# Optimization experiments

Measured on AMD Instinct MI355X. Metric: run time of the kernel, lower is better.

## Reference

```python
import jax, jax.numpy as jnp
import numpy as np


def _shared_mlp(x, W, s, b):
    # 1x1 conv over channel dim (last axis) + folded BN (scale/shift) + ReLU
    # x: (..., Cin), W: (Cout, Cin), s/b: (Cout,)
    return jax.nn.relu(jnp.einsum('...c,oc->...o', x, W) * s + b)


def setup_inputs() -> dict:
    key = jax.random.key(0)
    ks = jax.random.split(key, 15)
    B, N, K, C = 4, 4096, 32, 64
    D1, D2, DH = 64, 64, 128
    sc = 0.1
    return {
        'xyz': jax.random.normal(ks[0], (B, N, 3), dtype=jnp.float32),
        'features': jax.random.normal(ks[1], (B, C, N), dtype=jnp.float32),
        'idx': jax.random.randint(ks[2], (N, K), 0, N, dtype=jnp.int32),
        'W_gu': jax.random.normal(ks[3], (D1, 6), dtype=jnp.float32) * sc,
        's_gu': jnp.ones((D1,), jnp.float32),
        'b_gu': jax.random.normal(ks[4], (D1,), dtype=jnp.float32) * sc,
        'W_gv': jax.random.normal(ks[5], (D2, C), dtype=jnp.float32) * sc,
        's_gv': jnp.ones((D2,), jnp.float32),
        'b_gv': jax.random.normal(ks[6], (D2,), dtype=jnp.float32) * sc,
        'W_h': jax.random.normal(ks[7], (DH, D1 + D2), dtype=jnp.float32) * sc,
        's_h': jnp.ones((DH,), jnp.float32),
        'b_h': jax.random.normal(ks[8], (DH,), dtype=jnp.float32) * sc,
        'W_f': jax.random.normal(ks[9], (C, DH), dtype=jnp.float32) * sc,
        's_f': jnp.ones((C,), jnp.float32),
        'b_f': jax.random.normal(ks[10], (C,), dtype=jnp.float32) * sc,
    }


def reference(xyz, features, idx, W_gu, s_gu, b_gu, W_gv, s_gv, b_gv,
              W_h, s_h, b_h, W_f, s_f, b_f):
    # xyz: (B,N,3), features: (B,C,N), idx: (N,K) neighbor indices per point
    feats = jnp.swapaxes(features, 1, 2)              # (B,N,C)
    xyz_nb = xyz[:, idx, :]                           # (B,N,K,3) random gather
    feat_nb = feats[:, idx, :]                        # (B,N,K,C)
    K = idx.shape[1]
    center_xyz = jnp.broadcast_to(xyz[:, :, None, :], xyz_nb.shape)
    rel_xyz = jnp.concatenate([center_xyz, xyz_nb], axis=-1)   # (B,N,K,6)
    rel_feat = feat_nb + feats[:, :, None, :]                  # (B,N,K,C)

    gu = _shared_mlp(rel_xyz, W_gu, s_gu, b_gu)       # (B,N,K,D1)
    gv = _shared_mlp(rel_feat, W_gv, s_gv, b_gv)      # (B,N,K,D2)
    fuse = jnp.concatenate([gu, gv], axis=-1)         # (B,N,K,D1+D2)
    h = _shared_mlp(fuse, W_h, s_h, b_h)              # (B,N,K,DH)
    pooled = jnp.mean(h, axis=2)                      # (B,N,DH) mean over K
    out = _shared_mlp(pooled, W_f, s_f, b_f)          # (B,N,C)
    out = jnp.swapaxes(out, 1, 2) + features          # (B,C,N) residual
    return (xyz, out)
```

## Files before the change

### kernel.cpp

```cpp
#include <hip/hip_runtime.h>

#define B_  4
#define N_  4096
#define K_  32
#define C_  64
#define DH_ 128
#define PPB 16

typedef _Float16 half2v __attribute__((ext_vector_type(2)));
typedef _Float16 half8  __attribute__((ext_vector_type(8)));
typedef __fp16   fp16x2 __attribute__((ext_vector_type(2)));
typedef float  floatx16 __attribute__((ext_vector_type(16)));
typedef unsigned int uint_t;

union HU { half2v h; uint_t u; };
union HU2 { fp16x2 h; uint_t u; };

__device__ __forceinline__ uint_t pk2(float a, float b) {
    HU2 x; x.h = __builtin_amdgcn_cvt_pkrtz(a, b);
    return x.u;
}

__global__ __launch_bounds__(256) void k_transforms(
    const float* __restrict__ xyz,
    const float* __restrict__ W_h,
    const float* __restrict__ s_h,
    float* __restrict__ out_xyz,
    _Float16* __restrict__ Bpack)
{
    int e = blockIdx.x * 256 + threadIdx.x;
    if (e < B_*N_*3) { out_xyz[e] = xyz[e]; return; }
    e -= B_*N_*3;
    int j = e & 7, l = (e >> 3) & 63, c = (e >> 9) & 7, ob = e >> 12;
    int o = ob*32 + (l & 31);
    int i = c*16 + (l >> 5)*8 + j;
    Bpack[e] = (_Float16)(W_h[o*DH_ + i] * s_h[o]);
}

__global__ __launch_bounds__(256) void k_pre(
    const float* __restrict__ xyz,
    const float* __restrict__ features,
    const float* __restrict__ W_gv,
    const float* __restrict__ W_gu,
    const float* __restrict__ s_gu, const float* __restrict__ b_gu,
    const float* __restrict__ s_gv, const float* __restrict__ b_gv,
    uint_t* __restrict__ QsH,
    uint_t* __restrict__ PcatH)
{
    const int b  = blockIdx.x >> 6;
    const int n0 = (blockIdx.x & 63) * 64;
    const int t  = threadIdx.x;

    __shared__ __align__(16) float ftile[64 * 66];
    __shared__ __align__(16) float wtile[64 * 68];
    __shared__ float xs[192];
    __shared__ float wgu[384];

    const int nn = t & 63, cq = t >> 6;
#pragma unroll
    for (int r = 0; r < 16; r++) {
        int c = cq * 16 + r;
        ftile[c*66 + nn] = features[(b*C_ + c)*N_ + n0 + nn];
    }
    for (int e = t; e < 64*64; e += 256) {
        int o = e >> 6, c = e & 63;
        wtile[c*68 + o] = W_gv[e];
    }
    if (t < 192) xs[t] = xyz[(b*N_ + n0)*3 + t];
    if (t < 128) { wgu[t] = W_gu[t]; wgu[t+128] = W_gu[t+128]; wgu[t+256] = W_gu[t+256]; }
    __syncthreads();

    const int nt = t & 31, ot = t >> 5;
    const int nl0 = nt * 2, o0 = ot * 8;

    float acc[2][8] = {};
    for (int c = 0; c < 64; c++) {
        const float2 a = *(const float2*)&ftile[c*66 + nl0];
        float wv[8];
        *(float4*)&wv[0] = *(const float4*)&wtile[c*68 + o0];
        *(float4*)&wv[4] = *(const float4*)&wtile[c*68 + o0 + 4];
#pragma unroll
        for (int oo = 0; oo < 8; oo++) {
            acc[0][oo] = fmaf(a.x, wv[oo], acc[0][oo]);
            acc[1][oo] = fmaf(a.y, wv[oo], acc[1][oo]);
        }
    }

    float sgu[8], bgu[8], sgv[8], bgv[8];
    *(float4*)&sgu[0] = *(const float4*)&s_gu[o0]; *(float4*)&sgu[4] = *(const float4*)&s_gu[o0+4];
    *(float4*)&bgu[0] = *(const float4*)&b_gu[o0]; *(float4*)&bgu[4] = *(const float4*)&b_gu[o0+4];
    *(float4*)&sgv[0] = *(const float4*)&s_gv[o0]; *(float4*)&sgv[4] = *(const float4*)&s_gv[o0+4];
    *(float4*)&bgv[0] = *(const float4*)&b_gv[o0]; *(float4*)&bgv[4] = *(const float4*)&b_gv[o0+4];

#pragma unroll
    for (int kk = 0; kk < 2; kk++) {
        const int nl = nl0 + kk;
        const int bn = b*N_ + n0 + nl;
        const float x0 = xs[nl*3], x1 = xs[nl*3+1], x2 = xs[nl*3+2];
        float qv[8], rv[8];
#pragma unroll
        for (int oo = 0; oo < 8; oo++) {
            const int o = o0 + oo;
            qv[oo] = x0*wgu[o*6+0] + x1*wgu[o*6+1] + x2*wgu[o*6+2];
            rv[oo] = x0*wgu[o*6+3] + x1*wgu[o*6+4] + x2*wgu[o*6+5];
        }
        uint4 qa, pa;
        qa.x = pk2(qv[0]*sgu[0]+bgu[0], qv[1]*sgu[1]+bgu[1]);
        qa.y = pk2(qv[2]*sgu[2]+bgu[2], qv[3]*sgu[3]+bgu[3]);
        qa.z = pk2(qv[4]*sgu[4]+bgu[4], qv[5]*sgu[5]+bgu[5]);
        qa.w = pk2(qv[6]*sgu[6]+bgu[6], qv[7]*sgu[7]+bgu[7]);
        pa.x = pk2(rv[0]*sgu[0], rv[1]*sgu[1]);
        pa.y = pk2(rv[2]*sgu[2], rv[3]*sgu[3]);
        pa.z = pk2(rv[4]*sgu[4], rv[5]*sgu[5]);
        pa.w = pk2(rv[6]*sgu[6], rv[7]*sgu[7]);
        *(uint4*)&QsH  [bn*64 + ot*4] = qa;
        *(uint4*)&PcatH[bn*64 + ot*4] = pa;
        qa.x = pk2(acc[kk][0]*sgv[0]+bgv[0], acc[kk][1]*sgv[1]+bgv[1]);
        qa.y = pk2(acc[kk][2]*sgv[2]+bgv[2], acc[kk][3]*sgv[3]+bgv[3]);
        qa.z = pk2(acc[kk][4]*sgv[4]+bgv[4], acc[kk][5]*sgv[5]+bgv[5]);
        qa.w = pk2(acc[kk][6]*sgv[6]+bgv[6], acc[kk][7]*sgv[7]+bgv[7]);
        pa.x = pk2(acc[kk][0]*sgv[0], acc[kk][1]*sgv[1]);
        pa.y = pk2(acc[kk][2]*sgv[2], acc[kk][3]*sgv[3]);
        pa.z = pk2(acc[kk][4]*sgv[4], acc[kk][5]*sgv[5]);
        pa.w = pk2(acc[kk][6]*sgv[6], acc[kk][7]*sgv[7]);
        *(uint4*)&QsH  [bn*64 + 32 + ot*4] = qa;
        *(uint4*)&PcatH[bn*64 + 32 + ot*4] = pa;
    }
}

__global__ __launch_bounds__(256) void k_main(
    const int*      __restrict__ idx,
    const uint_t*   __restrict__ QsH,
    const uint_t*   __restrict__ PcatH,
    const _Float16* __restrict__ Bpack,
    const float*    __restrict__ b_h,
    const float*    __restrict__ W_f,
    const float*    __restrict__ s_f, const float* __restrict__ b_f,
    const float*    __restrict__ features,
    float* __restrict__ outF)
{
    const int t    = threadIdx.x;
    const int w    = t >> 6;
    const int lane = t & 63;
    const int m    = lane & 31;
    const int hh   = lane >> 5;
    const int slot = w >> 1;
    const int oh   = w & 1;

    __shared__ uint_t fuse[2 * 32 * 66];
    __shared__ __align__(16) float pooledAll[PPB * 136];

    half8 Bf[2][8];
#pragma unroll
    for (int ob = 0; ob < 2; ob++)
#pragma unroll
        for (int c = 0; c < 8; c++)
            Bf[ob][c] = *(const half8*)&Bpack[(((oh*2 + ob)*8 + c)*64 + lane)*8];

    const float bh0 = b_h[(oh*2+0)*32 + m];
    const float bh1 = b_h[(oh*2+1)*32 + m];

    const int bnb   = blockIdx.x * PPB;
    const int base0 = bnb & ~(N_ - 1);
    const half2v zero2 = {(_Float16)0.f, (_Float16)0.f};

    for (int rr = 0; rr < PPB/2; rr++) {
        const int bn0 = bnb + rr*2;
        const int jall = idx[((bn0 + hh) & (N_-1))*K_ + m];
        const uint_t qw0 = QsH[(bn0+0)*64 + lane];
        const uint_t qw1 = QsH[(bn0+1)*64 + lane];

        __syncthreads();
#pragma unroll
        for (int it = 0; it < 16; it++) {
            const int rs  = it*4 + w;
            const int sl  = rs >> 5, row = rs & 31;
            const int j   = __shfl(jall, rs);
            const uint_t rp = PcatH[(base0 + j)*64 + lane];
            HU a, p; a.u = sl ? qw1 : qw0; p.u = rp;
            half2v v = a.h + p.h;
            v = __builtin_elementwise_max(v, zero2);
            HU o2; o2.h = v;
            fuse[sl*2112 + row*66 + lane] = o2.u;
        }
        __syncthreads();

        floatx16 acc0 = {}, acc1 = {};
#pragma unroll
        for (int c = 0; c < 8; c++) {
            const int wb = slot*2112 + m*66 + c*8 + hh*4;
            union { uint_t u[4]; half8 h; } av;
            *(uint2*)&av.u[0] = *(const uint2*)&fuse[wb];
            *(uint2*)&av.u[2] = *(const uint2*)&fuse[wb + 2];
            acc0 = __builtin_amdgcn_mfma_f32_32x32x16_f16(av.h, Bf[0][c], acc0, 0, 0, 0);
            acc1 = __builtin_amdgcn_mfma_f32_32x32x16_f16(av.h, Bf[1][c], acc1, 0, 0, 0);
        }

        float v0 = 0.f, v1 = 0.f;
#pragma unroll
        for (int rg = 0; rg < 16; rg++) {
            v0 += fmaxf(acc0[rg] + bh0, 0.f);
            v1 += fmaxf(acc1[rg] + bh1, 0.f);
        }
        v0 += __shfl_xor(v0, 32);
        v1 += __shfl_xor(v1, 32);
        const int nl = rr*2 + slot;
        if (hh == 0) {
            pooledAll[nl*136 + (oh*2+0)*32 + m] = v0;
            pooledAll[nl*136 + (oh*2+1)*32 + m] = v1;
        }
    }
    __syncthreads();

    const int b  = bnb >> 12;
    const int n0 = bnb & (N_ - 1);
    const int c  = t >> 2;
    const int nq = t & 3;

    float acc[4] = {};
    for (int i0 = 0; i0 < DH_; i0 += 4) {
        const float4 wv = *(const float4*)&W_f[c*DH_ + i0];
#pragma unroll
        for (int r = 0; r < 4; r++) {
            const float4 p = *(const float4*)&pooledAll[(nq*4 + r)*136 + i0];
            acc[r] += wv.x*p.x + wv.y*p.y + wv.z*p.z + wv.w*p.w;
        }
    }
    const float sfc = s_f[c] * (1.f/(float)K_);
    const float bfc = b_f[c];
    const float4 fr = *(const float4*)&features[(b*C_ + c)*N_ + n0 + nq*4];
    float4 ov;
    ov.x = fmaxf(acc[0]*sfc + bfc, 0.f) + fr.x;
    ov.y = fmaxf(acc[1]*sfc + bfc, 0.f) + fr.y;
    ov.z = fmaxf(acc[2]*sfc + bfc, 0.f) + fr.z;
    ov.w = fmaxf(acc[3]*sfc + bfc, 0.f) + fr.w;
    *(float4*)&outF[(b*C_ + c)*N_ + n0 + nq*4] = ov;
}

extern "C" void kernel_launch(void* const* d_in, const int* in_sizes, int n_in,
                              void* d_out, int out_size, void* d_ws, size_t ws_size,
                              hipStream_t stream)
{
    const float* xyz      = (const float*)d_in[0];
    const float* features = (const float*)d_in[1];
    const int*   idx      = (const int*)  d_in[2];
    const float* W_gu     = (const float*)d_in[3];
    const float* s_gu     = (const float*)d_in[4];
    const float* b_gu     = (const float*)d_in[5];
    const float* W_gv     = (const float*)d_in[6];
    const float* s_gv     = (const float*)d_in[7];
    const float* b_gv     = (const float*)d_in[8];
    const float* W_h      = (const float*)d_in[9];
    const float* s_h      = (const float*)d_in[10];
    const float* b_h      = (const float*)d_in[11];
    const float* W_f      = (const float*)d_in[12];
    const float* s_f      = (const float*)d_in[13];
    const float* b_f      = (const float*)d_in[14];

    float* out  = (float*)d_out;
    float* outF = out + B_*N_*3;

    char* wp = (char*)d_ws;
    uint_t*   QsH   = (uint_t*)wp;   wp += (size_t)B_*N_*64*4;
    uint_t*   PcatH = (uint_t*)wp;   wp += (size_t)B_*N_*64*4;
    _Float16* Bpack = (_Float16*)wp; wp += DH_*(DH_)*2;

    k_transforms<<<256, 256, 0, stream>>>(xyz, W_h, s_h, out, Bpack);
    k_pre<<<B_*(N_/64), 256, 0, stream>>>(xyz, features, W_gv, W_gu,
                                          s_gu, b_gu, s_gv, b_gv, QsH, PcatH);
    k_main<<<(B_*N_)/PPB, 256, 0, stream>>>(idx, QsH, PcatH, Bpack, b_h,
                                            W_f, s_f, b_f, features, outF);
}
```

Before: 137.9 us.

## Gather neighbor rows directly into MFMA operands and shrink pre-kernel tiles

The main kernel no longer stages the gathered, ReLU-fused neighbor rows through shared memory with barriers. Each lane now loads its own neighbor's Pcat slice and the center Q slice straight from global memory and forms the MFMA A-operand in registers, with the two wave pairs each handling alternating points. The pre-kernel is re-tiled to 16 points per block with 4 outputs per thread, giving four times as many blocks. This removes LDS traffic and per-iteration syncs, but the gathers become 16-byte reads per lane at scattered addresses and the Q rows are re-read by every lane.

```diff
diff --git a/kernel.cpp b/kernel.cpp
--- a/kernel.cpp
+++ b/kernel.cpp
@@ -47,85 +47,69 @@
     uint_t* __restrict__ QsH,
     uint_t* __restrict__ PcatH)
 {
-    const int b  = blockIdx.x >> 6;
-    const int n0 = (blockIdx.x & 63) * 64;
+    const int b  = blockIdx.x >> 8;
+    const int n0 = (blockIdx.x & 255) * 16;
     const int t  = threadIdx.x;
 
-    __shared__ __align__(16) float ftile[64 * 66];
+    __shared__ __align__(16) float ftile[64 * 17];
     __shared__ __align__(16) float wtile[64 * 68];
-    __shared__ float xs[192];
-    __shared__ float wgu[384];
-
-    const int nn = t & 63, cq = t >> 6;
-#pragma unroll
-    for (int r = 0; r < 16; r++) {
-        int c = cq * 16 + r;
-        ftile[c*66 + nn] = features[(b*C_ + c)*N_ + n0 + nn];
+
+    {
+        const int c = t >> 2, nq = t & 3;
+        float4 f4 = *(const float4*)&features[(b*C_ + c)*N_ + n0 + nq*4];
+        ftile[c*17 + nq*4 + 0] = f4.x;
+        ftile[c*17 + nq*4 + 1] = f4.y;
+        ftile[c*17 + nq*4 + 2] = f4.z;
+        ftile[c*17 + nq*4 + 3] = f4.w;
     }
     for (int e = t; e < 64*64; e += 256) {
         int o = e >> 6, c = e & 63;
         wtile[c*68 + o] = W_gv[e];
     }
-    if (t < 192) xs[t] = xyz[(b*N_ + n0)*3 + t];
-    if (t < 128) { wgu[t] = W_gu[t]; wgu[t+128] = W_gu[t+128]; wgu[t+256] = W_gu[t+256]; }
     __syncthreads();
 
-    const int nt = t & 31, ot = t >> 5;
-    const int nl0 = nt * 2, o0 = ot * 8;
-
-    float acc[2][8] = {};
+    const int n  = t >> 4;
+    const int oq = t & 15;
+    const int o0 = oq * 4;
+
+    float acc[4] = {};
     for (int c = 0; c < 64; c++) {
-        const float2 a = *(const float2*)&ftile[c*66 + nl0];
-        float wv[8];
-        *(float4*)&wv[0] = *(const float4*)&wtile[c*68 + o0];
-        *(float4*)&wv[4] = *(const float4*)&wtile[c*68 + o0 + 4];
-#pragma unroll
-        for (int oo = 0; oo < 8; oo++) {
-            acc[0][oo] = fmaf(a.x, wv[oo], acc[0][oo]);
-            acc[1][oo] = fmaf(a.y, wv[oo], acc[1][oo]);
-        }
-    }
-
-    float sgu[8], bgu[8], sgv[8], bgv[8];
-    *(float4*)&sgu[0] = *(const float4*)&s_gu[o0]; *(float4*)&sgu[4] = *(const float4*)&s_gu[o0+4];
-    *(float4*)&bgu[0] = *(const float4*)&b_gu[o0]; *(float4*)&bgu[4] = *(const float4*)&b_gu[o0+4];
-    *(float4*)&sgv[0] = *(const float4*)&s_gv[o0]; *(float4*)&sgv[4] = *(const float4*)&s_gv[o0+4];
-    *(float4*)&bgv[0] = *(const float4*)&b_gv[o0]; *(float4*)&bgv[4] = *(const float4*)&b_gv[o0+4];
-
-#pragma unroll
-    for (int kk = 0; kk < 2; kk++) {
-        const int nl = nl0 + kk;
-        const int bn = b*N_ + n0 + nl;
-        const float x0 = xs[nl*3], x1 = xs[nl*3+1], x2 = xs[nl*3+2];
-        float qv[8], rv[8];
-#pragma unroll
-        for (int oo = 0; oo < 8; oo++) {
-            const int o = o0 + oo;
-            qv[oo] = x0*wgu[o*6+0] + x1*wgu[o*6+1] + x2*wgu[o*6+2];
-            rv[oo] = x0*wgu[o*6+3] + x1*wgu[o*6+4] + x2*wgu[o*6+5];
-        }
-        uint4 qa, pa;
-        qa.x = pk2(qv[0]*sgu[0]+bgu[0], qv[1]*sgu[1]+bgu[1]);
-        qa.y = pk2(qv[2]*sgu[2]+bgu[2], qv[3]*sgu[3]+bgu[3]);
-        qa.z = pk2(qv[4]*sgu[4]+bgu[4], qv[5]*sgu[5]+bgu[5]);
-        qa.w = pk2(qv[6]*sgu[6]+bgu[6], qv[7]*sgu[7]+bgu[7]);
-        pa.x = pk2(rv[0]*sgu[0], rv[1]*sgu[1]);
-        pa.y = pk2(rv[2]*sgu[2], rv[3]*sgu[3]);
-        pa.z = pk2(rv[4]*sgu[4], rv[5]*sgu[5]);
-        pa.w = pk2(rv[6]*sgu[6], rv[7]*sgu[7]);
-        *(uint4*)&QsH  [bn*64 + ot*4] = qa;
-        *(uint4*)&PcatH[bn*64 + ot*4] = pa;
-        qa.x = pk2(acc[kk][0]*sgv[0]+bgv[0], acc[kk][1]*sgv[1]+bgv[1]);
-        qa.y = pk2(acc[kk][2]*sgv[2]+bgv[2], acc[kk][3]*sgv[3]+bgv[3]);
-        qa.z = pk2(acc[kk][4]*sgv[4]+bgv[4], acc[kk][5]*sgv[5]+bgv[5]);
-        qa.w = pk2(acc[kk][6]*sgv[6]+bgv[6], acc[kk][7]*sgv[7]+bgv[7]);
-        pa.x = pk2(acc[kk][0]*sgv[0], acc[kk][1]*sgv[1]);
-        pa.y = pk2(acc[kk][2]*sgv[2], acc[kk][3]*sgv[3]);
-        pa.z = pk2(acc[kk][4]*sgv[4], acc[kk][5]*sgv[5]);
-        pa.w = pk2(acc[kk][6]*sgv[6], acc[kk][7]*sgv[7]);
-        *(uint4*)&QsH  [bn*64 + 32 + ot*4] = qa;
-        *(uint4*)&PcatH[bn*64 + 32 + ot*4] = pa;
-    }
+        const float a = ftile[c*17 + n];
+        const float4 wv = *(const float4*)&wtile[c*68 + o0];
+        acc[0] = fmaf(a, wv.x, acc[0]);
+        acc[1] = fmaf(a, wv.y, acc[1]);
+        acc[2] = fmaf(a, wv.z, acc[2]);
+        acc[3] = fmaf(a, wv.w, acc[3]);
+    }
+
+    const int bn = b*N_ + n0 + n;
+    const float x0 = xyz[bn*3+0], x1 = xyz[bn*3+1], x2 = xyz[bn*3+2];
+
+    const float4 sgu = *(const float4*)&s_gu[o0];
+    const float4 bgu = *(const float4*)&b_gu[o0];
+    const float4 sgv = *(const float4*)&s_gv[o0];
+    const float4 bgv = *(const float4*)&b_gv[o0];
+
+    float q[4], r[4];
+#pragma unroll
+    for (int jj = 0; jj < 4; jj++) {
+        const int o = o0 + jj;
+        q[jj] = x0*W_gu[o*6+0] + x1*W_gu[o*6+1] + x2*W_gu[o*6+2];
+        r[jj] = x0*W_gu[o*6+3] + x1*W_gu[o*6+4] + x2*W_gu[o*6+5];
+    }
+    uint2 qa, pa;
+    qa.x = pk2(q[0]*sgu.x+bgu.x, q[1]*sgu.y+bgu.y);
+    qa.y = pk2(q[2]*sgu.z+bgu.z, q[3]*sgu.w+bgu.w);
+    pa.x = pk2(r[0]*sgu.x, r[1]*sgu.y);
+    pa.y = pk2(r[2]*sgu.z, r[3]*sgu.w);
+    *(uint2*)&QsH  [bn*64 + oq*2] = qa;
+    *(uint2*)&PcatH[bn*64 + oq*2] = pa;
+    qa.x = pk2(acc[0]*sgv.x+bgv.x, acc[1]*sgv.y+bgv.y);
+    qa.y = pk2(acc[2]*sgv.z+bgv.z, acc[3]*sgv.w+bgv.w);
+    pa.x = pk2(acc[0]*sgv.x, acc[1]*sgv.y);
+    pa.y = pk2(acc[2]*sgv.z, acc[3]*sgv.w);
+    *(uint2*)&QsH  [bn*64 + 32 + oq*2] = qa;
+    *(uint2*)&PcatH[bn*64 + 32 + oq*2] = pa;
 }
 
 __global__ __launch_bounds__(256) void k_main(
@@ -147,7 +131,6 @@
     const int slot = w >> 1;
     const int oh   = w & 1;
 
-    __shared__ uint_t fuse[2 * 32 * 66];
     __shared__ __align__(16) float pooledAll[PPB * 136];
 
     half8 Bf[2][8];
@@ -164,34 +147,28 @@
     const int base0 = bnb & ~(N_ - 1);
     const half2v zero2 = {(_Float16)0.f, (_Float16)0.f};
 
-    for (int rr = 0; rr < PPB/2; rr++) {
-        const int bn0 = bnb + rr*2;
-        const int jall = idx[((bn0 + hh) & (N_-1))*K_ + m];
-        const uint_t qw0 = QsH[(bn0+0)*64 + lane];
-        const uint_t qw1 = QsH[(bn0+1)*64 + lane];
-
-        __syncthreads();
-#pragma unroll
-        for (int it = 0; it < 16; it++) {
-            const int rs  = it*4 + w;
-            const int sl  = rs >> 5, row = rs & 31;
-            const int j   = __shfl(jall, rs);
-            const uint_t rp = PcatH[(base0 + j)*64 + lane];
-            HU a, p; a.u = sl ? qw1 : qw0; p.u = rp;
-            half2v v = a.h + p.h;
-            v = __builtin_elementwise_max(v, zero2);
-            HU o2; o2.h = v;
-            fuse[sl*2112 + row*66 + lane] = o2.u;
-        }
-        __syncthreads();
+    for (int pp = slot; pp < PPB; pp += 2) {
+        const int bn = bnb + pp;
+        const int n  = bn & (N_ - 1);
+        const int j  = idx[n*K_ + m];
+        const uint_t* Pb = PcatH + (size_t)(base0 + j)*64 + hh*4;
+        const uint_t* Qb = QsH   + (size_t)bn*64 + hh*4;
 
         floatx16 acc0 = {}, acc1 = {};
 #pragma unroll
         for (int c = 0; c < 8; c++) {
-            const int wb = slot*2112 + m*66 + c*8 + hh*4;
+            const uint4 p4 = *(const uint4*)(Pb + c*8);
+            const uint4 q4 = *(const uint4*)(Qb + c*8);
             union { uint_t u[4]; half8 h; } av;
-            *(uint2*)&av.u[0] = *(const uint2*)&fuse[wb];
-            *(uint2*)&av.u[2] = *(const uint2*)&fuse[wb + 2];
+#pragma unroll
+            for (int qq = 0; qq < 4; qq++) {
+                HU a, p;
+                a.u = (&q4.x)[qq]; p.u = (&p4.x)[qq];
+                half2v v = a.h + p.h;
+                v = __builtin_elementwise_max(v, zero2);
+                HU o2; o2.h = v;
+                av.u[qq] = o2.u;
+            }
             acc0 = __builtin_amdgcn_mfma_f32_32x32x16_f16(av.h, Bf[0][c], acc0, 0, 0, 0);
             acc1 = __builtin_amdgcn_mfma_f32_32x32x16_f16(av.h, Bf[1][c], acc1, 0, 0, 0);
         }
@@ -204,10 +181,9 @@
         }
         v0 += __shfl_xor(v0, 32);
         v1 += __shfl_xor(v1, 32);
-        const int nl = rr*2 + slot;
         if (hh == 0) {
-            pooledAll[nl*136 + (oh*2+0)*32 + m] = v0;
-            pooledAll[nl*136 + (oh*2+1)*32 + m] = v1;
+            pooledAll[pp*136 + (oh*2+0)*32 + m] = v0;
+            pooledAll[pp*136 + (oh*2+1)*32 + m] = v1;
         }
     }
     __syncthreads();
@@ -263,10 +239,10 @@
     char* wp = (char*)d_ws;
     uint_t*   QsH   = (uint_t*)wp;   wp += (size_t)B_*N_*64*4;
     uint_t*   PcatH = (uint_t*)wp;   wp += (size_t)B_*N_*64*4;
-    _Float16* Bpack = (_Float16*)wp; wp += DH_*(DH_)*2;
+    _Float16* Bpack = (_Float16*)wp; wp += DH_*DH_*2;
 
     k_transforms<<<256, 256, 0, stream>>>(xyz, W_h, s_h, out, Bpack);
-    k_pre<<<B_*(N_/64), 256, 0, stream>>>(xyz, features, W_gv, W_gu,
+    k_pre<<<B_*(N_/16), 256, 0, stream>>>(xyz, features, W_gv, W_gu,
                                           s_gu, b_gu, s_gv, b_gv, QsH, PcatH);
     k_main<<<(B_*N_)/PPB, 256, 0, stream>>>(idx, QsH, PcatH, Bpack, b_h,
                                             W_f, s_f, b_f, features, outF);
```

Result: slower. 150.4 us (+9.1%).

## Merge transform and pre kernels; software-prefetch neighbor gathers in main loop

Applied to the files above, without the earlier changes.

Folds the xyz copy and W_h packing into the pre-compute kernel, which now launches twice as many blocks with 32 points each and reads W_gu straight from global memory. This removes one kernel launch and aims for better occupancy. The main kernel now loads all neighbor indices up front and prefetches the next point pair's PcatH gathers into registers while the current pair is being fused. This is meant to hide random-gather latency behind the MFMA work. It adds register pressure from 16 prefetched values plus 8 index registers, and the pooled row stride changes from 136 to 132.

```diff
diff --git a/kernel.cpp b/kernel.cpp
--- a/kernel.cpp
+++ b/kernel.cpp
@@ -21,70 +21,75 @@
     return x.u;
 }
 
-__global__ __launch_bounds__(256) void k_transforms(
-    const float* __restrict__ xyz,
-    const float* __restrict__ W_h,
-    const float* __restrict__ s_h,
-    float* __restrict__ out_xyz,
-    _Float16* __restrict__ Bpack)
-{
-    int e = blockIdx.x * 256 + threadIdx.x;
-    if (e < B_*N_*3) { out_xyz[e] = xyz[e]; return; }
-    e -= B_*N_*3;
-    int j = e & 7, l = (e >> 3) & 63, c = (e >> 9) & 7, ob = e >> 12;
-    int o = ob*32 + (l & 31);
-    int i = c*16 + (l >> 5)*8 + j;
-    Bpack[e] = (_Float16)(W_h[o*DH_ + i] * s_h[o]);
-}
-
-__global__ __launch_bounds__(256) void k_pre(
+__global__ __launch_bounds__(256) void k_prep(
     const float* __restrict__ xyz,
     const float* __restrict__ features,
     const float* __restrict__ W_gv,
     const float* __restrict__ W_gu,
     const float* __restrict__ s_gu, const float* __restrict__ b_gu,
     const float* __restrict__ s_gv, const float* __restrict__ b_gv,
+    const float* __restrict__ W_h,  const float* __restrict__ s_h,
+    float* __restrict__ out_xyz,
+    _Float16* __restrict__ Bpack,
     uint_t* __restrict__ QsH,
     uint_t* __restrict__ PcatH)
 {
-    const int b  = blockIdx.x >> 6;
-    const int n0 = (blockIdx.x & 63) * 64;
-    const int t  = threadIdx.x;
-
-    __shared__ __align__(16) float ftile[64 * 66];
+    const int blk = blockIdx.x;
+    const int b   = blk >> 7;
+    const int n0  = (blk & 127) * 32;
+    const int t   = threadIdx.x;
+
+    if (t < 96) { int e = blk*96 + t; out_xyz[e] = xyz[e]; }
+    {
+        int e = blk*32 + t;
+        if (t < 32) {
+            int j = e & 7, l = (e >> 3) & 63, c = (e >> 9) & 7, ob = e >> 12;
+            int o = ob*32 + (l & 31);
+            int i = c*16 + (l >> 5)*8 + j;
+            Bpack[e] = (_Float16)(W_h[o*DH_ + i] * s_h[o]);
+        }
+    }
+
+    __shared__ __align__(16) float ftile[64 * 33];
     __shared__ __align__(16) float wtile[64 * 68];
-    __shared__ float xs[192];
-    __shared__ float wgu[384];
-
-    const int nn = t & 63, cq = t >> 6;
-#pragma unroll
-    for (int r = 0; r < 16; r++) {
-        int c = cq * 16 + r;
-        ftile[c*66 + nn] = features[(b*C_ + c)*N_ + n0 + nn];
-    }
-    for (int e = t; e < 64*64; e += 256) {
-        int o = e >> 6, c = e & 63;
-        wtile[c*68 + o] = W_gv[e];
-    }
-    if (t < 192) xs[t] = xyz[(b*N_ + n0)*3 + t];
-    if (t < 128) { wgu[t] = W_gu[t]; wgu[t+128] = W_gu[t+128]; wgu[t+256] = W_gu[t+256]; }
+
+#pragma unroll
+    for (int r = 0; r < 2; r++) {
+        const int i4 = r*256 + t, c = i4 >> 3, nq = i4 & 7;
+        const float4 f4 = *(const float4*)&features[(b*C_ + c)*N_ + n0 + nq*4];
+        ftile[c*33 + nq*4 + 0] = f4.x;
+        ftile[c*33 + nq*4 + 1] = f4.y;
+        ftile[c*33 + nq*4 + 2] = f4.z;
+        ftile[c*33 + nq*4 + 3] = f4.w;
+    }
+#pragma unroll
+    for (int r = 0; r < 4; r++) {
+        const int e4 = r*256 + t, o = e4 >> 4, c0 = (e4 & 15)*4;
+        const float4 w4 = *(const float4*)&W_gv[o*C_ + c0];
+        wtile[(c0+0)*68 + o] = w4.x;
+        wtile[(c0+1)*68 + o] = w4.y;
+        wtile[(c0+2)*68 + o] = w4.z;
+        wtile[(c0+3)*68 + o] = w4.w;
+    }
     __syncthreads();
 
-    const int nt = t & 31, ot = t >> 5;
-    const int nl0 = nt * 2, o0 = ot * 8;
-
-    float acc[2][8] = {};
+    const int n  = t >> 3;
+    const int og = t & 7;
+    const int o0 = og * 8;
+
+    float acc[8] = {};
     for (int c = 0; c < 64; c++) {
-        const float2 a = *(const float2*)&ftile[c*66 + nl0];
+        const float a = ftile[c*33 + n];
         float wv[8];
         *(float4*)&wv[0] = *(const float4*)&wtile[c*68 + o0];
         *(float4*)&wv[4] = *(const float4*)&wtile[c*68 + o0 + 4];
 #pragma unroll
-        for (int oo = 0; oo < 8; oo++) {
-            acc[0][oo] = fmaf(a.x, wv[oo], acc[0][oo]);
-            acc[1][oo] = fmaf(a.y, wv[oo], acc[1][oo]);
-        }
-    }
+        for (int oo = 0; oo < 8; oo++)
+            acc[oo] = fmaf(a, wv[oo], acc[oo]);
+    }
+
+    const int bn = b*N_ + n0 + n;
+    const float x0 = xyz[bn*3+0], x1 = xyz[bn*3+1], x2 = xyz[bn*3+2];
 
     float sgu[8], bgu[8], sgv[8], bgv[8];
     *(float4*)&sgu[0] = *(const float4*)&s_gu[o0]; *(float4*)&sgu[4] = *(const float4*)&s_gu[o0+4];
@@ -92,40 +97,34 @@
     *(float4*)&sgv[0] = *(const float4*)&s_gv[o0]; *(float4*)&sgv[4] = *(const float4*)&s_gv[o0+4];
     *(float4*)&bgv[0] = *(const float4*)&b_gv[o0]; *(float4*)&bgv[4] = *(const float4*)&b_gv[o0+4];
 
-#pragma unroll
-    for (int kk = 0; kk < 2; kk++) {
-        const int nl = nl0 + kk;
-        const int bn = b*N_ + n0 + nl;
-        const float x0 = xs[nl*3], x1 = xs[nl*3+1], x2 = xs[nl*3+2];
-        float qv[8], rv[8];
-#pragma unroll
-        for (int oo = 0; oo < 8; oo++) {
-            const int o = o0 + oo;
-            qv[oo] = x0*wgu[o*6+0] + x1*wgu[o*6+1] + x2*wgu[o*6+2];
-            rv[oo] = x0*wgu[o*6+3] + x1*wgu[o*6+4] + x2*wgu[o*6+5];
-        }
-        uint4 qa, pa;
-        qa.x = pk2(qv[0]*sgu[0]+bgu[0], qv[1]*sgu[1]+bgu[1]);
-        qa.y = pk2(qv[2]*sgu[2]+bgu[2], qv[3]*sgu[3]+bgu[3]);
-        qa.z = pk2(qv[4]*sgu[4]+bgu[4], qv[5]*sgu[5]+bgu[5]);
-        qa.w = pk2(qv[6]*sgu[6]+bgu[6], qv[7]*sgu[7]+bgu[7]);
-        pa.x = pk2(rv[0]*sgu[0], rv[1]*sgu[1]);
-        pa.y = pk2(rv[2]*sgu[2], rv[3]*sgu[3]);
-        pa.z = pk2(rv[4]*sgu[4], rv[5]*sgu[5]);
-        pa.w = pk2(rv[6]*sgu[6], rv[7]*sgu[7]);
-        *(uint4*)&QsH  [bn*64 + ot*4] = qa;
-        *(uint4*)&PcatH[bn*64 + ot*4] = pa;
-        qa.x = pk2(acc[kk][0]*sgv[0]+bgv[0], acc[kk][1]*sgv[1]+bgv[1]);
-        qa.y = pk2(acc[kk][2]*sgv[2]+bgv[2], acc[kk][3]*sgv[3]+bgv[3]);
-        qa.z = pk2(acc[kk][4]*sgv[4]+bgv[4], acc[kk][5]*sgv[5]+bgv[5]);
-        qa.w = pk2(acc[kk][6]*sgv[6]+bgv[6], acc[kk][7]*sgv[7]+bgv[7]);
-        pa.x = pk2(acc[kk][0]*sgv[0], acc[kk][1]*sgv[1]);
-        pa.y = pk2(acc[kk][2]*sgv[2], acc[kk][3]*sgv[3]);
-        pa.z = pk2(acc[kk][4]*sgv[4], acc[kk][5]*sgv[5]);
-        pa.w = pk2(acc[kk][6]*sgv[6], acc[kk][7]*sgv[7]);
-        *(uint4*)&QsH  [bn*64 + 32 + ot*4] = qa;
-        *(uint4*)&PcatH[bn*64 + 32 + ot*4] = pa;
-    }
+    float qv[8], rv[8];
+#pragma unroll
+    for (int oo = 0; oo < 8; oo++) {
+        const int o = o0 + oo;
+        qv[oo] = x0*W_gu[o*6+0] + x1*W_gu[o*6+1] + x2*W_gu[o*6+2];
+        rv[oo] = x0*W_gu[o*6+3] + x1*W_gu[o*6+4] + x2*W_gu[o*6+5];
+    }
+    uint4 qa, pa;
+    qa.x = pk2(qv[0]*sgu[0]+bgu[0], qv[1]*sgu[1]+bgu[1]);
+    qa.y = pk2(qv[2]*sgu[2]+bgu[2], qv[3]*sgu[3]+bgu[3]);
+    qa.z = pk2(qv[4]*sgu[4]+bgu[4], qv[5]*sgu[5]+bgu[5]);
+    qa.w = pk2(qv[6]*sgu[6]+bgu[6], qv[7]*sgu[7]+bgu[7]);
+    pa.x = pk2(rv[0]*sgu[0], rv[1]*sgu[1]);
+    pa.y = pk2(rv[2]*sgu[2], rv[3]*sgu[3]);
+    pa.z = pk2(rv[4]*sgu[4], rv[5]*sgu[5]);
+    pa.w = pk2(rv[6]*sgu[6], rv[7]*sgu[7]);
+    *(uint4*)&QsH  [bn*64 + og*4] = qa;
+    *(uint4*)&PcatH[bn*64 + og*4] = pa;
+    qa.x = pk2(acc[0]*sgv[0]+bgv[0], acc[1]*sgv[1]+bgv[1]);
+    qa.y = pk2(acc[2]*sgv[2]+bgv[2], acc[3]*sgv[3]+bgv[3]);
+    qa.z = pk2(acc[4]*sgv[4]+bgv[4], acc[5]*sgv[5]+bgv[5]);
+    qa.w = pk2(acc[6]*sgv[6]+bgv[6], acc[7]*sgv[7]+bgv[7]);
+    pa.x = pk2(acc[0]*sgv[0], acc[1]*sgv[1]);
+    pa.y = pk2(acc[2]*sgv[2], acc[3]*sgv[3]);
+    pa.z = pk2(acc[4]*sgv[4], acc[5]*sgv[5]);
+    pa.w = pk2(acc[6]*sgv[6], acc[7]*sgv[7]);
+    *(uint4*)&QsH  [bn*64 + 32 + og*4] = qa;
+    *(uint4*)&PcatH[bn*64 + 32 + og*4] = pa;
 }
 
 __global__ __launch_bounds__(256) void k_main(
@@ -148,7 +147,7 @@
     const int oh   = w & 1;
 
     __shared__ uint_t fuse[2 * 32 * 66];
-    __shared__ __align__(16) float pooledAll[PPB * 136];
+    __shared__ __align__(16) float pooledAll[PPB * 132];
 
     half8 Bf[2][8];
 #pragma unroll
@@ -164,24 +163,43 @@
     const int base0 = bnb & ~(N_ - 1);
     const half2v zero2 = {(_Float16)0.f, (_Float16)0.f};
 
+    int jallv[PPB/2];
+#pragma unroll
+    for (int r = 0; r < PPB/2; r++)
+        jallv[r] = idx[((bnb + r*2 + hh) & (N_-1))*K_ + m];
+
+    uint_t qw0 = QsH[(bnb+0)*64 + lane];
+    uint_t qw1 = QsH[(bnb+1)*64 + lane];
+    uint_t pg[16];
+#pragma unroll
+    for (int it = 0; it < 16; it++) {
+        const int rs = it*4 + w;
+        const int j  = __shfl(jallv[0], rs);
+        pg[it] = PcatH[(size_t)(base0 + j)*64 + lane];
+    }
+
+#pragma unroll
     for (int rr = 0; rr < PPB/2; rr++) {
-        const int bn0 = bnb + rr*2;
-        const int jall = idx[((bn0 + hh) & (N_-1))*K_ + m];
-        const uint_t qw0 = QsH[(bn0+0)*64 + lane];
-        const uint_t qw1 = QsH[(bn0+1)*64 + lane];
-
-        __syncthreads();
 #pragma unroll
         for (int it = 0; it < 16; it++) {
             const int rs  = it*4 + w;
             const int sl  = rs >> 5, row = rs & 31;
-            const int j   = __shfl(jall, rs);
-            const uint_t rp = PcatH[(base0 + j)*64 + lane];
-            HU a, p; a.u = sl ? qw1 : qw0; p.u = rp;
+            HU a, p; a.u = sl ? qw1 : qw0; p.u = pg[it];
             half2v v = a.h + p.h;
             v = __builtin_elementwise_max(v, zero2);
             HU o2; o2.h = v;
             fuse[sl*2112 + row*66 + lane] = o2.u;
+        }
+        if (rr + 1 < PPB/2) {
+            const int bn0n = bnb + (rr+1)*2;
+            qw0 = QsH[(bn0n+0)*64 + lane];
+            qw1 = QsH[(bn0n+1)*64 + lane];
+#pragma unroll
+            for (int it = 0; it < 16; it++) {
+                const int rs = it*4 + w;
+                const int j  = __shfl(jallv[rr+1], rs);
+                pg[it] = PcatH[(size_t)(base0 + j)*64 + lane];
+            }
         }
         __syncthreads();
 
@@ -206,11 +224,11 @@
         v1 += __shfl_xor(v1, 32);
         const int nl = rr*2 + slot;
         if (hh == 0) {
-            pooledAll[nl*136 + (oh*2+0)*32 + m] = v0;
-            pooledAll[nl*136 + (oh*2+1)*32 + m] = v1;
-        }
-    }
-    __syncthreads();
+            pooledAll[nl*132 + (oh*2+0)*32 + m] = v0;
+            pooledAll[nl*132 + (oh*2+1)*32 + m] = v1;
+        }
+        __syncthreads();
+    }
 
     const int b  = bnb >> 12;
     const int n0 = bnb & (N_ - 1);
@@ -222,7 +240,7 @@
         const float4 wv = *(const float4*)&W_f[c*DH_ + i0];
 #pragma unroll
         for (int r = 0; r < 4; r++) {
-            const float4 p = *(const float4*)&pooledAll[(nq*4 + r)*136 + i0];
+            const float4 p = *(const float4*)&pooledAll[(nq*4 + r)*132 + i0];
             acc[r] += wv.x*p.x + wv.y*p.y + wv.z*p.z + wv.w*p.w;
         }
     }
@@ -263,11 +281,11 @@
     char* wp = (char*)d_ws;
     uint_t*   QsH   = (uint_t*)wp;   wp += (size_t)B_*N_*64*4;
     uint_t*   PcatH = (uint_t*)wp;   wp += (size_t)B_*N_*64*4;
-    _Float16* Bpack = (_Float16*)wp; wp += DH_*(DH_)*2;
-
-    k_transforms<<<256, 256, 0, stream>>>(xyz, W_h, s_h, out, Bpack);
-    k_pre<<<B_*(N_/64), 256, 0, stream>>>(xyz, features, W_gv, W_gu,
-                                          s_gu, b_gu, s_gv, b_gv, QsH, PcatH);
+    _Float16* Bpack = (_Float16*)wp; wp += DH_*DH_*2;
+
+    k_prep<<<B_*(N_/32), 256, 0, stream>>>(xyz, features, W_gv, W_gu,
+                                           s_gu, b_gu, s_gv, b_gv, W_h, s_h,
+                                           out, Bpack, QsH, PcatH);
     k_main<<<(B_*N_)/PPB, 256, 0, stream>>>(idx, QsH, PcatH, Bpack, b_h,
                                             W_f, s_f, b_f, features, outF);
 }
```

Result: faster. 130.4 us (-5.4%).
